# Kernel optimization log

Measured on AMD Instinct MI355X. Metric: run time of the kernel, lower is better.

Reference implementation:

```python
import jax, jax.numpy as jnp
import numpy as np

BETA = 0.85
THR = 1.0
SLOPE = 25.0  # fast_sigmoid surrogate slope

@jax.custom_vjp
def spike_fn(v):
    # Heaviside fire with fast-sigmoid surrogate gradient (snntorch fast_sigmoid)
    return (v > 0).astype(v.dtype)

def _spike_fwd(v):
    return (v > 0).astype(v.dtype), v

def _spike_bwd(v, g):
    return (g / (SLOPE * jnp.abs(v) + 1.0) ** 2,)

spike_fn.defvjp(_spike_fwd, _spike_bwd)

def setup_inputs() -> dict:
    key = jax.random.key(0)
    k1, k2, k3, k4, k5 = jax.random.split(key, 5)
    B, T, IN, H = 32, 2048, 512, 256
    x = jax.random.normal(k1, (B, T, IN), dtype=jnp.float32)
    s_in = 1.0 / np.sqrt(IN)
    s_h = 1.0 / np.sqrt(H)
    W_in = jax.random.uniform(k2, (H, IN), jnp.float32, -s_in, s_in)
    b_in = jax.random.uniform(k3, (H,), jnp.float32, -s_in, s_in)
    V = jax.random.uniform(k4, (H, H), jnp.float32, -s_h, s_h)   # RLeaky recurrent linear
    b_rec = jax.random.uniform(k5, (H,), jnp.float32, -s_h, s_h)
    return {"x": x, "W_in": W_in, "b_in": b_in, "V": V, "b_rec": b_rec}

def reference(x, W_in, b_in, V, b_rec):
    B, T, _ = x.shape
    H = W_in.shape[0]
    # input projection for all timesteps at once: (B,T,H) -> (T,B,H)
    proj = jnp.einsum('bti,hi->bth', x, W_in) + b_in
    proj_t = jnp.transpose(proj, (1, 0, 2))

    def step(carry, p_t):
        spk, mem = carry
        input_ = p_t + spk                       # combined = proj[:,t] + spk
        rec = spk @ V.T + b_rec                   # RLeaky recurrent term
        reset = jax.lax.stop_gradient((mem > THR).astype(mem.dtype))
        mem = BETA * mem + input_ + rec - reset * THR  # subtract reset
        spk = spike_fn(mem - THR)
        return (spk, mem), spk

    init = (jnp.zeros((B, H), x.dtype), jnp.zeros((B, H), x.dtype))
    _, spikes = jax.lax.scan(step, init, proj_t)  # (T,B,H)
    return jnp.transpose(spikes, (1, 0, 2))       # (B,T,H)
```

## Files before the change

### kernel.cpp

```cpp
#include <hip/hip_runtime.h>
#include <cstddef>
#include <cstdint>

#define kB 32
#define kT 2048
#define kIn 512
#define kH 256
#define kBeta 0.85f
#define kThr 1.0f

#define N_SCAN kB
#define N_GEMM (kB * 8)
#define FLAGS_PER_B 8
#define TBURST 8

#define GBM 256
#define GBK 16
#define GLDA 260
#define SMEM_FLOATS (2 * GBK * GLDA)

#define SSTRIDE 260

__device__ __forceinline__ void wait_flag(int* f) {
    while (__hip_atomic_load(f, __ATOMIC_ACQUIRE, __HIP_MEMORY_SCOPE_AGENT) == 0) {
        __builtin_amdgcn_s_sleep(2);
    }
}

__device__ void gemm_body(const float* __restrict__ A,
                          const float* __restrict__ W,
                          const float* __restrict__ bias,
                          float* __restrict__ P,
                          int* flags, int gid, float* smem)
{
    float* As = smem;
    float* Bs = smem + GBK * GLDA;
    const int tid = threadIdx.x;
    const int b  = gid & 31;
    const int tt = gid >> 5;
    const int bm = b * kT + tt * GBM;
    const int tx = tid & 31;
    const int ty = tid >> 5;

    float acc[8][8];
#pragma unroll
    for (int i = 0; i < 8; ++i)
#pragma unroll
        for (int j = 0; j < 8; ++j) acc[i][j] = 0.f;

    const int r = tid >> 2, kc = (tid & 3) << 2;

    for (int kb = 0; kb < kIn; kb += GBK) {
        const float4 av = *reinterpret_cast<const float4*>(A + (size_t)(bm + r) * kIn + kb + kc);
        const float4 bv = *reinterpret_cast<const float4*>(W + (size_t)r * kIn + kb + kc);
        __syncthreads();
        As[(kc + 0) * GLDA + r] = av.x;
        As[(kc + 1) * GLDA + r] = av.y;
        As[(kc + 2) * GLDA + r] = av.z;
        As[(kc + 3) * GLDA + r] = av.w;
        Bs[(kc + 0) * GLDA + r] = bv.x;
        Bs[(kc + 1) * GLDA + r] = bv.y;
        Bs[(kc + 2) * GLDA + r] = bv.z;
        Bs[(kc + 3) * GLDA + r] = bv.w;
        __syncthreads();

#pragma unroll
        for (int k = 0; k < GBK; ++k) {
            const float4 aa0 = *reinterpret_cast<const float4*>(&As[k * GLDA + ty * 4]);
            const float4 aa1 = *reinterpret_cast<const float4*>(&As[k * GLDA + ty * 4 + 128]);
            const float4 bb0 = *reinterpret_cast<const float4*>(&Bs[k * GLDA + tx * 4]);
            const float4 bb1 = *reinterpret_cast<const float4*>(&Bs[k * GLDA + tx * 4 + 128]);
            const float av8[8] = {aa0.x, aa0.y, aa0.z, aa0.w, aa1.x, aa1.y, aa1.z, aa1.w};
            const float bv8[8] = {bb0.x, bb0.y, bb0.z, bb0.w, bb1.x, bb1.y, bb1.z, bb1.w};
#pragma unroll
            for (int i = 0; i < 8; ++i)
#pragma unroll
                for (int j = 0; j < 8; ++j)
                    acc[i][j] = fmaf(av8[i], bv8[j], acc[i][j]);
        }
    }

    const float4 bl = *reinterpret_cast<const float4*>(bias + tx * 4);
    const float4 bh = *reinterpret_cast<const float4*>(bias + tx * 4 + 128);
#pragma unroll
    for (int i = 0; i < 8; ++i) {
        const int m = bm + ty * 4 + (i & 3) + ((i >> 2) << 7);
        float4 o0, o1;
        o0.x = acc[i][0] + bl.x; o0.y = acc[i][1] + bl.y;
        o0.z = acc[i][2] + bl.z; o0.w = acc[i][3] + bl.w;
        o1.x = acc[i][4] + bh.x; o1.y = acc[i][5] + bh.y;
        o1.z = acc[i][6] + bh.z; o1.w = acc[i][7] + bh.w;
        *reinterpret_cast<float4*>(P + (size_t)m * kH + tx * 4) = o0;
        *reinterpret_cast<float4*>(P + (size_t)m * kH + tx * 4 + 128) = o1;
    }

    __syncthreads();
    if (flags && tid == 0) {
        __threadfence();
        atomicAdd(flags + b * FLAGS_PER_B + tt, 1);
    }
}

__device__ void scan_body(float* __restrict__ PO,
                          const float* __restrict__ V,
                          const float* __restrict__ brec,
                          int* flags, float* smem)
{
    unsigned long long* smask = reinterpret_cast<unsigned long long*>(smem);
    float* pbuf = smem + 16;

    const int b = blockIdx.x;
    const int tid = threadIdx.x;
    const int w = tid >> 6;
    const int l = tid & 63;
    const int h0 = l << 2;
    const int kc = w << 4;
    const bool owner = (tid < kH);
    const int h = tid & (kH - 1);

    float Vr[4][16];
#pragma unroll
    for (int i = 0; i < 4; ++i) {
        const float4* vp = reinterpret_cast<const float4*>(V + (size_t)(h0 + i) * kH + kc);
#pragma unroll
        for (int c4 = 0; c4 < 4; ++c4) {
            const float4 v = vp[c4];
            Vr[i][c4 * 4 + 0] = v.x; Vr[i][c4 * 4 + 1] = v.y;
            Vr[i][c4 * 4 + 2] = v.z; Vr[i][c4 * 4 + 3] = v.w;
        }
    }

    const float br = owner ? brec[h] : 0.f;
    float mem = 0.f, spk = 0.f;
    float* base = PO + (size_t)b * (size_t)kT * kH + h;

    if (tid < 4) smask[tid] = 0ull;

    int* bflags = flags ? (flags + b * FLAGS_PER_B) : nullptr;

    float pb[TBURST], pb2[TBURST], sst[TBURST];
    if (owner) {
        if (bflags) wait_flag(bflags + 0);
#pragma unroll
        for (int i = 0; i < TBURST; ++i) pb[i] = base[(size_t)i * kH];
    }
    __syncthreads();

    const int mshift = (w & 3) << 4;

    for (int tb = 0; tb < kT / TBURST; ++tb) {
#pragma unroll
        for (int ti = 0; ti < TBURST; ++ti) {

            if (owner && ti == 0) {
                if (tb > 0) {
#pragma unroll
                    for (int i = 0; i < TBURST; ++i)
                        base[(size_t)((tb - 1) * TBURST + i) * kH] = sst[i];
                }
                const int nb = tb + 1;
                if (bflags && nb < (kT / TBURST) && (nb & 31) == 0)
                    wait_flag(bflags + (nb >> 5));
#pragma unroll
                for (int i = 0; i < TBURST; ++i) {
                    int tt2 = nb * TBURST + i;
                    if (tt2 > kT - 1) tt2 = kT - 1;
                    pb2[i] = base[(size_t)tt2 * kH];
                }
            }

            const unsigned long long m = smask[w >> 2];
            const uint32_t chunk =
                __builtin_amdgcn_readfirstlane((uint32_t)(m >> mshift)) & 0xFFFFu;

            float a0 = 0.f, a1 = 0.f, a2 = 0.f, a3 = 0.f;
#pragma unroll
            for (int n = 0; n < 4; ++n) {
                const uint32_t nib = (chunk >> (n * 4)) & 0xFu;
                if (nib) {
#pragma unroll
                    for (int bit = 0; bit < 4; ++bit) {
                        const int j = n * 4 + bit;
                        const float bf = (float)((nib >> bit) & 1u);
                        a0 = fmaf(bf, Vr[0][j], a0);
                        a1 = fmaf(bf, Vr[1][j], a1);
                        a2 = fmaf(bf, Vr[2][j], a2);
                        a3 = fmaf(bf, Vr[3][j], a3);
                    }
                }
            }
            float4 part; part.x = a0; part.y = a1; part.z = a2; part.w = a3;
            *reinterpret_cast<float4*>(pbuf + w * SSTRIDE + h0) = part;

            __syncthreads();

            if (owner) {
                float s0  = pbuf[ 0 * SSTRIDE + h], s1  = pbuf[ 1 * SSTRIDE + h];
                float s2  = pbuf[ 2 * SSTRIDE + h], s3  = pbuf[ 3 * SSTRIDE + h];
                float s4  = pbuf[ 4 * SSTRIDE + h], s5  = pbuf[ 5 * SSTRIDE + h];
                float s6  = pbuf[ 6 * SSTRIDE + h], s7  = pbuf[ 7 * SSTRIDE + h];
                float s8  = pbuf[ 8 * SSTRIDE + h], s9  = pbuf[ 9 * SSTRIDE + h];
                float s10 = pbuf[10 * SSTRIDE + h], s11 = pbuf[11 * SSTRIDE + h];
                float s12 = pbuf[12 * SSTRIDE + h], s13 = pbuf[13 * SSTRIDE + h];
                float s14 = pbuf[14 * SSTRIDE + h], s15 = pbuf[15 * SSTRIDE + h];
                const float r0 = (s0 + s1) + (s2 + s3);
                const float r1 = (s4 + s5) + (s6 + s7);
                const float r2 = (s8 + s9) + (s10 + s11);
                const float r3 = (s12 + s13) + (s14 + s15);
                const float rec = ((r0 + r1) + (r2 + r3)) + br;
                const float p = pb[ti];
                float m2;
                {
#pragma clang fp contract(off)
                    const float input_ = p + spk;
                    m2 = kBeta * mem;
                    m2 = m2 + input_;
                    m2 = m2 + rec;
                    m2 = m2 - spk * kThr;
                }
                const bool fire = (m2 > kThr);
                const float ns = fire ? 1.0f : 0.0f;
                const unsigned long long bm = __ballot(fire);
                if ((tid & 63) == 0) smask[tid >> 6] = bm;
                mem = m2;
                spk = ns;
                sst[ti] = ns;
            }

            __syncthreads();
        }
        if (owner) {
#pragma unroll
            for (int i = 0; i < TBURST; ++i) pb[i] = pb2[i];
        }
    }

    if (owner) {
#pragma unroll
        for (int i = 0; i < TBURST; ++i)
            base[(size_t)((kT / TBURST - 1) * TBURST + i) * kH] = sst[i];
    }
}

__global__ void __launch_bounds__(1024, 4)
fused(const float* __restrict__ x, const float* __restrict__ W,
      const float* __restrict__ b_in, const float* __restrict__ V,
      const float* __restrict__ b_rec, float* __restrict__ PO,
      int* flags, int n_scan)
{
    __shared__ __align__(16) float smem[SMEM_FLOATS];
    if ((int)blockIdx.x < n_scan) {
        scan_body(PO, V, b_rec, flags, smem);
    } else {
        gemm_body(x, W, b_in, PO, flags, (int)blockIdx.x - n_scan, smem);
    }
}

extern "C" void kernel_launch(void* const* d_in, const int* in_sizes, int n_in,
                              void* d_out, int out_size, void* d_ws, size_t ws_size,
                              hipStream_t stream) {
    const float* x     = (const float*)d_in[0];
    const float* W_in  = (const float*)d_in[1];
    const float* b_in  = (const float*)d_in[2];
    const float* V     = (const float*)d_in[3];
    const float* b_rec = (const float*)d_in[4];
    float* out = (float*)d_out;

    const size_t flag_bytes = (size_t)N_SCAN * FLAGS_PER_B * sizeof(int);
    if (ws_size >= flag_bytes) {
        int* flags = (int*)d_ws;
        hipMemsetAsync(flags, 0, flag_bytes, stream);
        fused<<<N_SCAN + N_GEMM, 1024, 0, stream>>>(x, W_in, b_in, V, b_rec,
                                                    out, flags, N_SCAN);
    } else {
        fused<<<N_GEMM, 1024, 0, stream>>>(x, W_in, b_in, V, b_rec, out, nullptr, 0);
        fused<<<N_SCAN, 1024, 0, stream>>>(x, W_in, b_in, V, b_rec, out, nullptr, N_SCAN);
    }
}
```

Baseline: 1.750 ms.

## Shrink scan block to four waves with register-held V and single barrier per step

```diff
diff --git a/kernel.cpp b/kernel.cpp
--- a/kernel.cpp
+++ b/kernel.cpp
@@ -10,16 +10,15 @@
 #define kThr 1.0f
 
 #define N_SCAN kB
-#define N_GEMM (kB * 8)
-#define FLAGS_PER_B 8
+#define GEMM_TM 128
+#define N_TILES (kT / GEMM_TM)
+#define N_GEMM (kB * N_TILES)
+#define FLAGS_PER_B N_TILES
 #define TBURST 8
 
-#define GBM 256
-#define GBK 16
-#define GLDA 260
-#define SMEM_FLOATS (2 * GBK * GLDA)
-
-#define SSTRIDE 260
+#define ALD 132
+#define BLD 260
+#define SMEM_FLOATS (16 * ALD + 16 * BLD)
 
 __device__ __forceinline__ void wait_flag(int* f) {
     while (__hip_atomic_load(f, __ATOMIC_ACQUIRE, __HIP_MEMORY_SCOPE_AGENT) == 0) {
@@ -34,64 +33,88 @@
                           int* flags, int gid, float* smem)
 {
     float* As = smem;
-    float* Bs = smem + GBK * GLDA;
+    float* Bs = smem + 16 * ALD;
     const int tid = threadIdx.x;
     const int b  = gid & 31;
     const int tt = gid >> 5;
-    const int bm = b * kT + tt * GBM;
-    const int tx = tid & 31;
-    const int ty = tid >> 5;
-
-    float acc[8][8];
+    const int bm = b * kT + tt * GEMM_TM;
+    const int tx = tid & 15;
+    const int ty = tid >> 4;
+
+    float acc[8][16];
 #pragma unroll
     for (int i = 0; i < 8; ++i)
 #pragma unroll
-        for (int j = 0; j < 8; ++j) acc[i][j] = 0.f;
-
-    const int r = tid >> 2, kc = (tid & 3) << 2;
-
-    for (int kb = 0; kb < kIn; kb += GBK) {
-        const float4 av = *reinterpret_cast<const float4*>(A + (size_t)(bm + r) * kIn + kb + kc);
-        const float4 bv = *reinterpret_cast<const float4*>(W + (size_t)r * kIn + kb + kc);
+        for (int j = 0; j < 16; ++j) acc[i][j] = 0.f;
+
+    const int ra0 = tid >> 2,          ka0 = (tid & 3) << 2;
+    const int ra1 = (tid + 256) >> 2,  ka1 = (tid & 3) << 2;
+
+    for (int kb = 0; kb < kIn; kb += 16) {
+        const float4 a0 = *reinterpret_cast<const float4*>(A + (size_t)(bm + ra0) * kIn + kb + ka0);
+        const float4 a1 = *reinterpret_cast<const float4*>(A + (size_t)(bm + ra1) * kIn + kb + ka1);
+        float4 wv[4];
+#pragma unroll
+        for (int j = 0; j < 4; ++j) {
+            const int c = tid + 256 * j;
+            wv[j] = *reinterpret_cast<const float4*>(W + (size_t)(c >> 2) * kIn + kb + ((c & 3) << 2));
+        }
         __syncthreads();
-        As[(kc + 0) * GLDA + r] = av.x;
-        As[(kc + 1) * GLDA + r] = av.y;
-        As[(kc + 2) * GLDA + r] = av.z;
-        As[(kc + 3) * GLDA + r] = av.w;
-        Bs[(kc + 0) * GLDA + r] = bv.x;
-        Bs[(kc + 1) * GLDA + r] = bv.y;
-        Bs[(kc + 2) * GLDA + r] = bv.z;
-        Bs[(kc + 3) * GLDA + r] = bv.w;
+        As[(ka0 + 0) * ALD + ra0] = a0.x;
+        As[(ka0 + 1) * ALD + ra0] = a0.y;
+        As[(ka0 + 2) * ALD + ra0] = a0.z;
+        As[(ka0 + 3) * ALD + ra0] = a0.w;
+        As[(ka1 + 0) * ALD + ra1] = a1.x;
+        As[(ka1 + 1) * ALD + ra1] = a1.y;
+        As[(ka1 + 2) * ALD + ra1] = a1.z;
+        As[(ka1 + 3) * ALD + ra1] = a1.w;
+#pragma unroll
+        for (int j = 0; j < 4; ++j) {
+            const int c = tid + 256 * j;
+            const int rw = c >> 2, kw = (c & 3) << 2;
+            Bs[(kw + 0) * BLD + rw] = wv[j].x;
+            Bs[(kw + 1) * BLD + rw] = wv[j].y;
+            Bs[(kw + 2) * BLD + rw] = wv[j].z;
+            Bs[(kw + 3) * BLD + rw] = wv[j].w;
+        }
         __syncthreads();
 
 #pragma unroll
-        for (int k = 0; k < GBK; ++k) {
-            const float4 aa0 = *reinterpret_cast<const float4*>(&As[k * GLDA + ty * 4]);
-            const float4 aa1 = *reinterpret_cast<const float4*>(&As[k * GLDA + ty * 4 + 128]);
-            const float4 bb0 = *reinterpret_cast<const float4*>(&Bs[k * GLDA + tx * 4]);
-            const float4 bb1 = *reinterpret_cast<const float4*>(&Bs[k * GLDA + tx * 4 + 128]);
-            const float av8[8] = {aa0.x, aa0.y, aa0.z, aa0.w, aa1.x, aa1.y, aa1.z, aa1.w};
-            const float bv8[8] = {bb0.x, bb0.y, bb0.z, bb0.w, bb1.x, bb1.y, bb1.z, bb1.w};
+        for (int k = 0; k < 16; ++k) {
+            const float4 aa0 = *reinterpret_cast<const float4*>(&As[k * ALD + ty * 4]);
+            const float4 aa1 = *reinterpret_cast<const float4*>(&As[k * ALD + ty * 4 + 64]);
+            float av8[8] = {aa0.x, aa0.y, aa0.z, aa0.w, aa1.x, aa1.y, aa1.z, aa1.w};
+            float bv16[16];
+#pragma unroll
+            for (int g = 0; g < 4; ++g) {
+                const float4 bb = *reinterpret_cast<const float4*>(&Bs[k * BLD + tx * 4 + g * 64]);
+                bv16[g * 4 + 0] = bb.x; bv16[g * 4 + 1] = bb.y;
+                bv16[g * 4 + 2] = bb.z; bv16[g * 4 + 3] = bb.w;
+            }
 #pragma unroll
             for (int i = 0; i < 8; ++i)
 #pragma unroll
-                for (int j = 0; j < 8; ++j)
-                    acc[i][j] = fmaf(av8[i], bv8[j], acc[i][j]);
-        }
-    }
-
-    const float4 bl = *reinterpret_cast<const float4*>(bias + tx * 4);
-    const float4 bh = *reinterpret_cast<const float4*>(bias + tx * 4 + 128);
+                for (int j = 0; j < 16; ++j)
+                    acc[i][j] = fmaf(av8[i], bv16[j], acc[i][j]);
+        }
+    }
+
+    float4 bl[4];
+#pragma unroll
+    for (int g = 0; g < 4; ++g)
+        bl[g] = *reinterpret_cast<const float4*>(bias + tx * 4 + g * 64);
 #pragma unroll
     for (int i = 0; i < 8; ++i) {
-        const int m = bm + ty * 4 + (i & 3) + ((i >> 2) << 7);
-        float4 o0, o1;
-        o0.x = acc[i][0] + bl.x; o0.y = acc[i][1] + bl.y;
-        o0.z = acc[i][2] + bl.z; o0.w = acc[i][3] + bl.w;
-        o1.x = acc[i][4] + bh.x; o1.y = acc[i][5] + bh.y;
-        o1.z = acc[i][6] + bh.z; o1.w = acc[i][7] + bh.w;
-        *reinterpret_cast<float4*>(P + (size_t)m * kH + tx * 4) = o0;
-        *reinterpret_cast<float4*>(P + (size_t)m * kH + tx * 4 + 128) = o1;
+        const int m = bm + ty * 4 + (i & 3) + ((i >> 2) << 6);
+#pragma unroll
+        for (int g = 0; g < 4; ++g) {
+            float4 o;
+            o.x = acc[i][g * 4 + 0] + bl[g].x;
+            o.y = acc[i][g * 4 + 1] + bl[g].y;
+            o.z = acc[i][g * 4 + 2] + bl[g].z;
+            o.w = acc[i][g * 4 + 3] + bl[g].w;
+            *reinterpret_cast<float4*>(P + (size_t)m * kH + tx * 4 + g * 64) = o;
+        }
     }
 
     __syncthreads();
@@ -106,61 +129,53 @@
                           const float* __restrict__ brec,
                           int* flags, float* smem)
 {
-    unsigned long long* smask = reinterpret_cast<unsigned long long*>(smem);
-    float* pbuf = smem + 16;
+    float* pbuf0 = smem;
+    float* pbuf1 = smem + 1024;
 
     const int b = blockIdx.x;
     const int tid = threadIdx.x;
     const int w = tid >> 6;
     const int l = tid & 63;
     const int h0 = l << 2;
-    const int kc = w << 4;
-    const bool owner = (tid < kH);
-    const int h = tid & (kH - 1);
-
-    float Vr[4][16];
+
+    float Vr[4][64];
 #pragma unroll
     for (int i = 0; i < 4; ++i) {
-        const float4* vp = reinterpret_cast<const float4*>(V + (size_t)(h0 + i) * kH + kc);
-#pragma unroll
-        for (int c4 = 0; c4 < 4; ++c4) {
-            const float4 v = vp[c4];
-            Vr[i][c4 * 4 + 0] = v.x; Vr[i][c4 * 4 + 1] = v.y;
-            Vr[i][c4 * 4 + 2] = v.z; Vr[i][c4 * 4 + 3] = v.w;
-        }
-    }
-
-    const float br = owner ? brec[h] : 0.f;
+        const float4* vp = reinterpret_cast<const float4*>(V + (size_t)(h0 + i) * kH + (w << 6));
+#pragma unroll
+        for (int c = 0; c < 16; ++c) {
+            const float4 v = vp[c];
+            Vr[i][c * 4 + 0] = v.x; Vr[i][c * 4 + 1] = v.y;
+            Vr[i][c * 4 + 2] = v.z; Vr[i][c * 4 + 3] = v.w;
+        }
+    }
+
+    const float br = brec[tid];
     float mem = 0.f, spk = 0.f;
-    float* base = PO + (size_t)b * (size_t)kT * kH + h;
-
-    if (tid < 4) smask[tid] = 0ull;
+    unsigned long long bm = 0ull;
+    float* base = PO + (size_t)b * (size_t)kT * kH + tid;
 
     int* bflags = flags ? (flags + b * FLAGS_PER_B) : nullptr;
 
     float pb[TBURST], pb2[TBURST], sst[TBURST];
-    if (owner) {
-        if (bflags) wait_flag(bflags + 0);
-#pragma unroll
-        for (int i = 0; i < TBURST; ++i) pb[i] = base[(size_t)i * kH];
-    }
-    __syncthreads();
-
-    const int mshift = (w & 3) << 4;
+    if (bflags) wait_flag(bflags + 0);
+#pragma unroll
+    for (int i = 0; i < TBURST; ++i) pb[i] = base[(size_t)i * kH];
 
     for (int tb = 0; tb < kT / TBURST; ++tb) {
 #pragma unroll
         for (int ti = 0; ti < TBURST; ++ti) {
-
-            if (owner && ti == 0) {
+            const int t = tb * TBURST + ti;
+
+            if (ti == 0) {
                 if (tb > 0) {
 #pragma unroll
                     for (int i = 0; i < TBURST; ++i)
                         base[(size_t)((tb - 1) * TBURST + i) * kH] = sst[i];
                 }
                 const int nb = tb + 1;
-                if (bflags && nb < (kT / TBURST) && (nb & 31) == 0)
-                    wait_flag(bflags + (nb >> 5));
+                if (bflags && nb < (kT / TBURST) && (nb & 15) == 0)
+                    wait_flag(bflags + (nb >> 4));
 #pragma unroll
                 for (int i = 0; i < TBURST; ++i) {
                     int tt2 = nb * TBURST + i;
@@ -169,50 +184,52 @@
                 }
             }
 
-            const unsigned long long m = smask[w >> 2];
-            const uint32_t chunk =
-                __builtin_amdgcn_readfirstlane((uint32_t)(m >> mshift)) & 0xFFFFu;
-
-            float a0 = 0.f, a1 = 0.f, a2 = 0.f, a3 = 0.f;
-#pragma unroll
-            for (int n = 0; n < 4; ++n) {
-                const uint32_t nib = (chunk >> (n * 4)) & 0xFu;
+            float* pw = (t & 1) ? pbuf1 : pbuf0;
+
+            const uint32_t lo = (uint32_t)bm;
+            const uint32_t hi = (uint32_t)(bm >> 32);
+            float a[4][4];
+#pragma unroll
+            for (int i = 0; i < 4; ++i)
+#pragma unroll
+                for (int s = 0; s < 4; ++s) a[i][s] = 0.f;
+
+#pragma unroll
+            for (int n = 0; n < 16; ++n) {
+                const uint32_t nib = ((n < 8 ? lo : hi) >> ((n & 7) * 4)) & 0xFu;
                 if (nib) {
+                    const int s = n >> 2;
 #pragma unroll
                     for (int bit = 0; bit < 4; ++bit) {
-                        const int j = n * 4 + bit;
-                        const float bf = (float)((nib >> bit) & 1u);
-                        a0 = fmaf(bf, Vr[0][j], a0);
-                        a1 = fmaf(bf, Vr[1][j], a1);
-                        a2 = fmaf(bf, Vr[2][j], a2);
-                        a3 = fmaf(bf, Vr[3][j], a3);
+                        const int k = n * 4 + bit;
+                        const float bf = ((nib >> bit) & 1u) ? 1.0f : 0.0f;
+                        a[0][s] = fmaf(bf, Vr[0][k], a[0][s]);
+                        a[1][s] = fmaf(bf, Vr[1][k], a[1][s]);
+                        a[2][s] = fmaf(bf, Vr[2][k], a[2][s]);
+                        a[3][s] = fmaf(bf, Vr[3][k], a[3][s]);
                     }
                 }
             }
-            float4 part; part.x = a0; part.y = a1; part.z = a2; part.w = a3;
-            *reinterpret_cast<float4*>(pbuf + w * SSTRIDE + h0) = part;
+            float4 part;
+            part.x = (a[0][0] + a[0][1]) + (a[0][2] + a[0][3]);
+            part.y = (a[1][0] + a[1][1]) + (a[1][2] + a[1][3]);
+            part.z = (a[2][0] + a[2][1]) + (a[2][2] + a[2][3]);
+            part.w = (a[3][0] + a[3][1]) + (a[3][2] + a[3][3]);
+            *reinterpret_cast<float4*>(pw + w * kH + h0) = part;
 
             __syncthreads();
 
-            if (owner) {
-                float s0  = pbuf[ 0 * SSTRIDE + h], s1  = pbuf[ 1 * SSTRIDE + h];
-                float s2  = pbuf[ 2 * SSTRIDE + h], s3  = pbuf[ 3 * SSTRIDE + h];
-                float s4  = pbuf[ 4 * SSTRIDE + h], s5  = pbuf[ 5 * SSTRIDE + h];
-                float s6  = pbuf[ 6 * SSTRIDE + h], s7  = pbuf[ 7 * SSTRIDE + h];
-                float s8  = pbuf[ 8 * SSTRIDE + h], s9  = pbuf[ 9 * SSTRIDE + h];
-                float s10 = pbuf[10 * SSTRIDE + h], s11 = pbuf[11 * SSTRIDE + h];
-                float s12 = pbuf[12 * SSTRIDE + h], s13 = pbuf[13 * SSTRIDE + h];
-                float s14 = pbuf[14 * SSTRIDE + h], s15 = pbuf[15 * SSTRIDE + h];
-                const float r0 = (s0 + s1) + (s2 + s3);
-                const float r1 = (s4 + s5) + (s6 + s7);
-                const float r2 = (s8 + s9) + (s10 + s11);
-                const float r3 = (s12 + s13) + (s14 + s15);
-                const float rec = ((r0 + r1) + (r2 + r3)) + br;
-                const float p = pb[ti];
+            {
+                const float p0 = pw[0 * kH + tid];
+                const float p1 = pw[1 * kH + tid];
+                const float p2 = pw[2 * kH + tid];
+                const float p3 = pw[3 * kH + tid];
+                const float rec = ((p0 + p1) + (p2 + p3)) + br;
+                const float pj = pb[ti];
                 float m2;
                 {
 #pragma clang fp contract(off)
-                    const float input_ = p + spk;
+                    const float input_ = pj + spk;
                     m2 = kBeta * mem;
                     m2 = m2 + input_;
                     m2 = m2 + rec;
@@ -220,29 +237,22 @@
                 }
                 const bool fire = (m2 > kThr);
                 const float ns = fire ? 1.0f : 0.0f;
-                const unsigned long long bm = __ballot(fire);
-                if ((tid & 63) == 0) smask[tid >> 6] = bm;
+                bm = __ballot(fire);
                 mem = m2;
                 spk = ns;
                 sst[ti] = ns;
             }
-
-            __syncthreads();
-        }
-        if (owner) {
-#pragma unroll
-            for (int i = 0; i < TBURST; ++i) pb[i] = pb2[i];
-        }
-    }
-
-    if (owner) {
-#pragma unroll
-        for (int i = 0; i < TBURST; ++i)
-            base[(size_t)((kT / TBURST - 1) * TBURST + i) * kH] = sst[i];
-    }
-}
-
-__global__ void __launch_bounds__(1024, 4)
+        }
+#pragma unroll
+        for (int i = 0; i < TBURST; ++i) pb[i] = pb2[i];
+    }
+
+#pragma unroll
+    for (int i = 0; i < TBURST; ++i)
+        base[(size_t)((kT / TBURST - 1) * TBURST + i) * kH] = sst[i];
+}
+
+__global__ void __launch_bounds__(256, 1)
 fused(const float* __restrict__ x, const float* __restrict__ W,
       const float* __restrict__ b_in, const float* __restrict__ V,
       const float* __restrict__ b_rec, float* __restrict__ PO,
@@ -266,14 +276,14 @@
     const float* b_rec = (const float*)d_in[4];
     float* out = (float*)d_out;
 
-    const size_t flag_bytes = (size_t)N_SCAN * FLAGS_PER_B * sizeof(int);
+    const size_t flag_bytes = (size_t)kB * FLAGS_PER_B * sizeof(int);
     if (ws_size >= flag_bytes) {
         int* flags = (int*)d_ws;
         hipMemsetAsync(flags, 0, flag_bytes, stream);
-        fused<<<N_SCAN + N_GEMM, 1024, 0, stream>>>(x, W_in, b_in, V, b_rec,
-                                                    out, flags, N_SCAN);
+        fused<<<N_SCAN + N_GEMM, 256, 0, stream>>>(x, W_in, b_in, V, b_rec,
+                                                   out, flags, N_SCAN);
     } else {
-        fused<<<N_GEMM, 1024, 0, stream>>>(x, W_in, b_in, V, b_rec, out, nullptr, 0);
-        fused<<<N_SCAN, 1024, 0, stream>>>(x, W_in, b_in, V, b_rec, out, nullptr, N_SCAN);
-    }
-}
+        fused<<<N_GEMM, 256, 0, stream>>>(x, W_in, b_in, V, b_rec, out, nullptr, 0);
+        fused<<<N_SCAN, 256, 0, stream>>>(x, W_in, b_in, V, b_rec, out, nullptr, N_SCAN);
+    }
+}
```

Measured after the change: 2.236 ms. 1.28x slower.
